# Kernel optimization log

Hardware: AMD Instinct MI355X
Metric: run time of the kernel (lower is better)

## Reference

```python
import jax, jax.numpy as jnp
import numpy as np

NODE_DIM, EDGE_DIM = 128, 64
N_NODES, N_EDGES = 50000, 500000
BN_EPS = 1e-5


def _glorot(key, shape):
    fan_in, fan_out = shape[0], shape[-1]
    s = np.sqrt(2.0 / (fan_in + fan_out)).astype(np.float32)
    return jax.random.normal(key, shape, jnp.float32) * s


def setup_inputs() -> dict:
    key = jax.random.key(0)
    ks = jax.random.split(key, 24)
    inp = {
        "x": jax.random.normal(ks[0], (N_NODES, NODE_DIM), jnp.float32),
        "edge_index": jax.random.randint(ks[1], (2, N_EDGES), 0, N_NODES),
        "edge_features": jax.random.normal(ks[2], (N_EDGES, EDGE_DIM), jnp.float32),
        "num_nodes": N_NODES,
        # CustomSAGEConv params (shared across the num_layers loop, as the module
        # instantiates a single self.conv)
        "W_nb": _glorot(ks[3], (NODE_DIM + EDGE_DIM, NODE_DIM)),
        "b_nb": jnp.zeros((NODE_DIM,), jnp.float32),
        "W_self": _glorot(ks[4], (NODE_DIM, NODE_DIM)),
        "b_self": jnp.zeros((NODE_DIM,), jnp.float32),
    }
    # MLP: 320 -> 512 -> 256 -> 128 -> 64 -> 32 -> 1, BN after first two linears
    dims = [2 * NODE_DIM + EDGE_DIM, 512, 256, 128, 64, 32, 1]
    for i in range(6):
        inp[f"W{i+1}"] = _glorot(ks[5 + i], (dims[i], dims[i + 1]))
        inp[f"b{i+1}"] = jnp.zeros((dims[i + 1],), jnp.float32)
    inp["g1"] = jnp.ones((512,), jnp.float32)
    inp["beta1"] = jnp.zeros((512,), jnp.float32)
    inp["g2"] = jnp.ones((256,), jnp.float32)
    inp["beta2"] = jnp.zeros((256,), jnp.float32)
    return inp


def _batchnorm(h, g, b):
    # training-mode batch statistics (deterministic reference)
    m = jnp.mean(h, axis=0)
    v = jnp.var(h, axis=0)
    return g * (h - m) * jax.lax.rsqrt(v + BN_EPS) + b


def _sage_conv(x, src, dst, ef, num_nodes, W_nb, b_nb, W_self, b_self):
    # message from source node + edge feature, mean-aggregated at destination
    msg = jnp.concatenate([x[src], ef], axis=-1) @ W_nb + b_nb  # [E, node_dim]
    deg = jax.ops.segment_sum(jnp.ones(src.shape[0], x.dtype), dst, num_segments=num_nodes)
    agg = jax.ops.segment_sum(msg, dst, num_segments=num_nodes) / jnp.clip(deg, 1.0)[:, None]
    return x @ W_self + b_self + agg


def reference(x, edge_index, edge_features, num_nodes,
              W_nb, b_nb, W_self, b_self,
              W1, b1, W2, b2, W3, b3, W4, b4, W5, b5, W6, b6,
              g1, beta1, g2, beta2):
    src, dst = edge_index[0], edge_index[1]
    num_layers = 2
    for _ in range(num_layers):
        x = _sage_conv(x, src, dst, edge_features, num_nodes, W_nb, b_nb, W_self, b_self)
        x = jax.nn.relu(x)  # dropout is identity in eval
    v, u = edge_index[0], edge_index[1]
    pair = jnp.concatenate([x[v], x[u], edge_features], axis=-1)  # [E, 320]
    h = jax.nn.relu(_batchnorm(pair @ W1 + b1, g1, beta1))
    h = jax.nn.relu(_batchnorm(h @ W2 + b2, g2, beta2))
    h = jax.nn.relu(h @ W3 + b3)
    h = jax.nn.relu(h @ W4 + b4)
    h = jax.nn.relu(h @ W5 + b5)
    return h @ W6 + b6  # [E, 1]
```

## Files before the change

kernel.cpp:

```cpp
#include <hip/hip_runtime.h>

using bf16 = __bf16;
typedef bf16 bf16x8 __attribute__((ext_vector_type(8)));
typedef float f32x4 __attribute__((ext_vector_type(4)));

#define MFMA16(a, b, c) __builtin_amdgcn_mfma_f32_16x16x32_bf16(a, b, c, 0, 0, 0)


__device__ __forceinline__ bf16x8 to_bf16x8(float4 a, float4 b) {
    bf16x8 v;
    v[0] = (bf16)a.x; v[1] = (bf16)a.y; v[2] = (bf16)a.z; v[3] = (bf16)a.w;
    v[4] = (bf16)b.x; v[5] = (bf16)b.y; v[6] = (bf16)b.z; v[7] = (bf16)b.w;
    return v;
}

__device__ __forceinline__ bf16x8 lds_afrag(const char* smem, int ldK, int mbase, int kbase, int lane) {
    int r = mbase + (lane & 15);
    int off = (kbase + ((lane >> 4) << 3)) << 1;
    off ^= (r & 7) << 4;
    return *(const bf16x8*)(smem + r * (ldK << 1) + off);
}

__device__ __forceinline__ bf16x8 glb_bfrag(const bf16* __restrict__ WT, int K, int nbase, int kbase, int lane) {
    int n = nbase + (lane & 15);
    int k = kbase + ((lane >> 4) << 3);
    return *(const bf16x8*)(WT + (size_t)n * K + k);
}


__global__ void k_transpose(const float* __restrict__ W, bf16* __restrict__ WT,
                            int K, int N, int ldT, int k0) {
    int idx = blockIdx.x * 256 + threadIdx.x;
    if (idx < K * N) {
        int k = idx / N, n = idx - k * N;
        WT[(size_t)n * ldT + k0 + k] = (bf16)W[idx];
    }
}

__global__ void k_deg(const int* __restrict__ dst, float* __restrict__ deg, int E) {
    int e = blockIdx.x * 256 + threadIdx.x;
    if (e < E) atomicAdd(&deg[dst[e]], 1.0f);
}

__global__ void k_scan(const float* __restrict__ deg, unsigned* __restrict__ offsets,
                       float* __restrict__ invdeg, int N) {
    __shared__ unsigned wsum[16];
    __shared__ unsigned carry_s, tot_s;
    const int tid = threadIdx.x, lane = tid & 63, wid = tid >> 6;
    if (tid == 0) carry_s = 0;
    __syncthreads();
    for (int base = 0; base < N; base += 1024) {
        int i = base + tid;
        unsigned v = (i < N) ? (unsigned)deg[i] : 0u;
        unsigned inc = v;
        #pragma unroll
        for (int d = 1; d < 64; d <<= 1) {
            unsigned t = (unsigned)__shfl_up((int)inc, d, 64);
            if (lane >= d) inc += t;
        }
        if (lane == 63) wsum[wid] = inc;
        __syncthreads();
        if (wid == 0) {
            unsigned wv = (lane < 16) ? wsum[lane] : 0u;
            unsigned winc = wv;
            #pragma unroll
            for (int d = 1; d < 16; d <<= 1) {
                unsigned t = (unsigned)__shfl_up((int)winc, d, 16);
                if ((lane & 15) >= d) winc += t;
            }
            if (lane < 16) wsum[lane] = winc - wv;
            if (lane == 15) tot_s = winc;
        }
        __syncthreads();
        if (i < N) {
            offsets[i] = carry_s + wsum[wid] + (inc - v);
            invdeg[i] = 1.0f / fmaxf(deg[i], 1.0f);
        }
        __syncthreads();
        if (tid == 0) carry_s += tot_s;
        __syncthreads();
    }
    if (tid == 0) offsets[N] = carry_s;
}

__global__ void k_scatter(const int* __restrict__ dst, const unsigned* __restrict__ offsets,
                          unsigned* __restrict__ cursor, unsigned* __restrict__ eid, int E) {
    int e = blockIdx.x * 256 + threadIdx.x;
    if (e < E) {
        int d = dst[e];
        unsigned p = atomicAdd(&cursor[d], 1u);
        eid[offsets[d] + p] = (unsigned)e;
    }
}

__global__ __launch_bounds__(256)
void k_agg(const float* __restrict__ xin, const float* __restrict__ ef, const int* __restrict__ src,
           const unsigned* __restrict__ offsets, const float* __restrict__ invdeg,
           const unsigned* __restrict__ eid, float* __restrict__ sm, int N) {
    const int lane = threadIdx.x & 63, w = threadIdx.x >> 6;
    int nb = blockIdx.x * 16 + w * 4;
    for (int j = 0; j < 4; ++j) {
        int n = nb + j;
        if (n >= N) return;
        unsigned o0 = offsets[n], o1 = offsets[n + 1];
        float s0 = 0.f, s1 = 0.f, s2 = 0.f;
        for (unsigned t = o0; t < o1; ++t) {
            int e = (int)eid[t];
            int v = src[e];
            s0 += xin[(size_t)v * 128 + lane];
            s1 += xin[(size_t)v * 128 + 64 + lane];
            s2 += ef[(size_t)e * 64 + lane];
        }
        float g = invdeg[n];
        sm[(size_t)n * 192 + lane] = s0 * g;
        sm[(size_t)n * 192 + 64 + lane] = s1 * g;
        sm[(size_t)n * 192 + 128 + lane] = s2 * g;
    }
}

__global__ __launch_bounds__(256)
void k_nodegemm(const float* __restrict__ xin, const float* __restrict__ sm,
                const bf16* __restrict__ WcatT,
                const float* __restrict__ b_self, const float* __restrict__ b_nb,
                const unsigned* __restrict__ offsets,
                float* __restrict__ xout, int N) {
    __shared__ char smem[64 * 320 * 2];
    const int tid = threadIdx.x, lane = tid & 63, w = tid >> 6;
    const int n0 = blockIdx.x * 64;
    for (int it = tid; it < 64 * 40; it += 256) {
        int r = it / 40, c = it - r * 40;
        int node = n0 + r;
        float4 fa = {0, 0, 0, 0}, fb = {0, 0, 0, 0};
        if (node < N) {
            int base = c * 8;
            const float* p = (base < 128) ? xin + (size_t)node * 128 + base
                                          : sm + (size_t)node * 192 + (base - 128);
            fa = *(const float4*)p;
            fb = *(const float4*)(p + 4);
        }
        bf16x8 v = to_bf16x8(fa, fb);
        *(bf16x8*)(smem + r * 640 + ((c * 16) ^ ((r & 7) << 4))) = v;
    }
    __syncthreads();

    f32x4 acc[4][2];
    #pragma unroll
    for (int m = 0; m < 4; ++m)
        #pragma unroll
        for (int n = 0; n < 2; ++n) acc[m][n] = (f32x4){0.f, 0.f, 0.f, 0.f};

    for (int ks = 0; ks < 10; ++ks) {
        bf16x8 a[4];
        #pragma unroll
        for (int m = 0; m < 4; ++m) a[m] = lds_afrag(smem, 320, m * 16, ks * 32, lane);
        #pragma unroll
        for (int n = 0; n < 2; ++n) {
            bf16x8 b = glb_bfrag(WcatT, 320, w * 32 + n * 16, ks * 32, lane);
            #pragma unroll
            for (int m = 0; m < 4; ++m) acc[m][n] = MFMA16(a[m], b, acc[m][n]);
        }
    }

    #pragma unroll
    for (int n = 0; n < 2; ++n) {
        int col = w * 32 + n * 16 + (lane & 15);
        float bs = b_self[col], bn = b_nb[col];
        #pragma unroll
        for (int m = 0; m < 4; ++m)
            #pragma unroll
            for (int rr = 0; rr < 4; ++rr) {
                int row = m * 16 + ((lane >> 4) << 2) + rr;
                int node = n0 + row;
                if (node < N) {
                    bool hd = offsets[node + 1] > offsets[node];
                    xout[(size_t)node * 128 + col] =
                        fmaxf(acc[m][n][rr] + bs + (hd ? bn : 0.f), 0.f);
                }
            }
    }
}

__global__ void k_finalize(const float* __restrict__ sum, const float* __restrict__ sq,
                           const float* __restrict__ g, const float* __restrict__ beta,
                           float* __restrict__ scale, float* __restrict__ shift,
                           int n, float invE) {
    int i = blockIdx.x * 256 + threadIdx.x;
    if (i < n) {
        float m = sum[i] * invE;
        float v = sq[i] * invE - m * m;
        float sc = g[i] * rsqrtf(v + 1e-5f);
        scale[i] = sc;
        shift[i] = beta[i] - m * sc;
    }
}

template <int PASS>
__global__ __launch_bounds__(256, 2)
void k_mlp(const float* __restrict__ x, const int* __restrict__ ei, const float* __restrict__ ef,
           const bf16* __restrict__ W1T, const float* __restrict__ b1,
           const bf16* __restrict__ W2T, const float* __restrict__ b2,
           const bf16* __restrict__ W3T, const float* __restrict__ b3,
           const bf16* __restrict__ W4T, const float* __restrict__ b4,
           const bf16* __restrict__ W5T, const float* __restrict__ b5,
           const float* __restrict__ W6, const float* __restrict__ b6,
           const float* __restrict__ scale1, const float* __restrict__ shift1,
           const float* __restrict__ scale2, const float* __restrict__ shift2,
           float* __restrict__ sum1, float* __restrict__ sq1,
           float* __restrict__ sum2, float* __restrict__ sq2,
           float* __restrict__ out, int E) {
    __shared__ char smem[65536];
    const int tid = threadIdx.x, lane = tid & 63, w = tid >> 6;
    const int e0 = blockIdx.x * 64;
    const int* src = ei;
    const int* dst = ei + E;

    for (int it = tid; it < 64 * 40; it += 256) {
        int r = it / 40, c = it - r * 40;
        int ge = e0 + r;
        float4 fa = {0, 0, 0, 0}, fb = {0, 0, 0, 0};
        if (ge < E) {
            int base = c * 8;
            const float* p;
            if (base < 128)      p = x + (size_t)src[ge] * 128 + base;
            else if (base < 256) p = x + (size_t)dst[ge] * 128 + (base - 128);
            else                 p = ef + (size_t)ge * 64 + (base - 256);
            fa = *(const float4*)p;
            fb = *(const float4*)(p + 4);
        }
        bf16x8 v = to_bf16x8(fa, fb);
        *(bf16x8*)(smem + r * 640 + ((c * 16) ^ ((r & 7) << 4))) = v;
    }
    __syncthreads();

    f32x4 acc[4][8];
    #pragma unroll
    for (int m = 0; m < 4; ++m)
        #pragma unroll
        for (int n = 0; n < 8; ++n) acc[m][n] = (f32x4){0.f, 0.f, 0.f, 0.f};
    #pragma unroll 2
    for (int ks = 0; ks < 10; ++ks) {
        bf16x8 a[4];
        #pragma unroll
        for (int m = 0; m < 4; ++m) a[m] = lds_afrag(smem, 320, m * 16, ks * 32, lane);
        #pragma unroll
        for (int n = 0; n < 8; ++n) {
            bf16x8 b = glb_bfrag(W1T, 320, w * 128 + n * 16, ks * 32, lane);
            #pragma unroll
            for (int m = 0; m < 4; ++m) acc[m][n] = MFMA16(a[m], b, acc[m][n]);
        }
    }
    const int cb = w * 128;

    if (PASS == 0) {
        #pragma unroll
        for (int n = 0; n < 8; ++n) {
            int col = cb + n * 16 + (lane & 15);
            float bb = b1[col];
            float s = 0.f, q = 0.f;
            #pragma unroll
            for (int m = 0; m < 4; ++m)
                #pragma unroll
                for (int rr = 0; rr < 4; ++rr) {
                    int row = m * 16 + ((lane >> 4) << 2) + rr;
                    if (e0 + row < E) {
                        float h = acc[m][n][rr] + bb;
                        s += h; q += h * h;
                    }
                }
            s += __shfl_xor(s, 16); s += __shfl_xor(s, 32);
            q += __shfl_xor(q, 16); q += __shfl_xor(q, 32);
            if (lane < 16) { atomicAdd(&sum1[col], s); atomicAdd(&sq1[col], q); }
        }
        return;
    }

    __syncthreads();
    #pragma unroll
    for (int n = 0; n < 8; ++n) {
        int col = cb + n * 16 + (lane & 15);
        float bb = b1[col], sc = scale1[col], sh = shift1[col];
        #pragma unroll
        for (int m = 0; m < 4; ++m)
            #pragma unroll
            for (int rr = 0; rr < 4; ++rr) {
                int row = m * 16 + ((lane >> 4) << 2) + rr;
                float a = fmaxf(fmaf(acc[m][n][rr] + bb, sc, sh), 0.f);
                int off = (col * 2) ^ ((row & 7) << 4);
                *(bf16*)(smem + row * 1024 + off) = (bf16)a;
            }
    }
    __syncthreads();

    f32x4 acc2[4][4];
    #pragma unroll
    for (int m = 0; m < 4; ++m)
        #pragma unroll
        for (int n = 0; n < 4; ++n) acc2[m][n] = (f32x4){0.f, 0.f, 0.f, 0.f};
    #pragma unroll 2
    for (int ks = 0; ks < 16; ++ks) {
        bf16x8 a[4];
        #pragma unroll
        for (int m = 0; m < 4; ++m) a[m] = lds_afrag(smem, 512, m * 16, ks * 32, lane);
        #pragma unroll
        for (int n = 0; n < 4; ++n) {
            bf16x8 b = glb_bfrag(W2T, 512, w * 64 + n * 16, ks * 32, lane);
            #pragma unroll
            for (int m = 0; m < 4; ++m) acc2[m][n] = MFMA16(a[m], b, acc2[m][n]);
        }
    }
    const int cb2 = w * 64;

    if (PASS == 1) {
        #pragma unroll
        for (int n = 0; n < 4; ++n) {
            int col = cb2 + n * 16 + (lane & 15);
            float bb = b2[col];
            float s = 0.f, q = 0.f;
            #pragma unroll
            for (int m = 0; m < 4; ++m)
                #pragma unroll
                for (int rr = 0; rr < 4; ++rr) {
                    int row = m * 16 + ((lane >> 4) << 2) + rr;
                    if (e0 + row < E) {
                        float h = acc2[m][n][rr] + bb;
                        s += h; q += h * h;
                    }
                }
            s += __shfl_xor(s, 16); s += __shfl_xor(s, 32);
            q += __shfl_xor(q, 16); q += __shfl_xor(q, 32);
            if (lane < 16) { atomicAdd(&sum2[col], s); atomicAdd(&sq2[col], q); }
        }
        return;
    }

    __syncthreads();
    if (tid < 32) *(float*)(smem + 49152 + tid * 4) = W6[tid];
    #pragma unroll
    for (int n = 0; n < 4; ++n) {
        int col = cb2 + n * 16 + (lane & 15);
        float bb = b2[col], sc = scale2[col], sh = shift2[col];
        #pragma unroll
        for (int m = 0; m < 4; ++m)
            #pragma unroll
            for (int rr = 0; rr < 4; ++rr) {
                int row = m * 16 + ((lane >> 4) << 2) + rr;
                float a = fmaxf(fmaf(acc2[m][n][rr] + bb, sc, sh), 0.f);
                int off = (col * 2) ^ ((row & 7) << 4);
                *(bf16*)(smem + row * 512 + off) = (bf16)a;
            }
    }
    __syncthreads();

    f32x4 acc3[4][2];
    #pragma unroll
    for (int m = 0; m < 4; ++m)
        #pragma unroll
        for (int n = 0; n < 2; ++n) acc3[m][n] = (f32x4){0.f, 0.f, 0.f, 0.f};
    for (int ks = 0; ks < 8; ++ks) {
        bf16x8 a[4];
        #pragma unroll
        for (int m = 0; m < 4; ++m) a[m] = lds_afrag(smem, 256, m * 16, ks * 32, lane);
        #pragma unroll
        for (int n = 0; n < 2; ++n) {
            bf16x8 b = glb_bfrag(W3T, 256, w * 32 + n * 16, ks * 32, lane);
            #pragma unroll
            for (int m = 0; m < 4; ++m) acc3[m][n] = MFMA16(a[m], b, acc3[m][n]);
        }
    }
    __syncthreads();
    #pragma unroll
    for (int n = 0; n < 2; ++n) {
        int col = w * 32 + n * 16 + (lane & 15);
        float bb = b3[col];
        #pragma unroll
        for (int m = 0; m < 4; ++m)
            #pragma unroll
            for (int rr = 0; rr < 4; ++rr) {
                int row = m * 16 + ((lane >> 4) << 2) + rr;
                float a = fmaxf(acc3[m][n][rr] + bb, 0.f);
                int off = (col * 2) ^ ((row & 7) << 4);
                *(bf16*)(smem + row * 256 + off) = (bf16)a;
            }
    }
    __syncthreads();

    f32x4 acc4[4];
    #pragma unroll
    for (int m = 0; m < 4; ++m) acc4[m] = (f32x4){0.f, 0.f, 0.f, 0.f};
    for (int ks = 0; ks < 4; ++ks) {
        bf16x8 a[4];
        #pragma unroll
        for (int m = 0; m < 4; ++m) a[m] = lds_afrag(smem, 128, m * 16, ks * 32, lane);
        bf16x8 b = glb_bfrag(W4T, 128, w * 16, ks * 32, lane);
        #pragma unroll
        for (int m = 0; m < 4; ++m) acc4[m] = MFMA16(a[m], b, acc4[m]);
    }
    __syncthreads();
    {
        int col = w * 16 + (lane & 15);
        float bb = b4[col];
        #pragma unroll
        for (int m = 0; m < 4; ++m)
            #pragma unroll
            for (int rr = 0; rr < 4; ++rr) {
                int row = m * 16 + ((lane >> 4) << 2) + rr;
                float a = fmaxf(acc4[m][rr] + bb, 0.f);
                int off = (col * 2) ^ ((row & 7) << 4);
                *(bf16*)(smem + row * 128 + off) = (bf16)a;
            }
    }
    __syncthreads();

    if (w < 2) {
        f32x4 acc5[4];
        #pragma unroll
        for (int m = 0; m < 4; ++m) acc5[m] = (f32x4){0.f, 0.f, 0.f, 0.f};
        for (int ks = 0; ks < 2; ++ks) {
            bf16x8 a[4];
            #pragma unroll
            for (int m = 0; m < 4; ++m) a[m] = lds_afrag(smem, 64, m * 16, ks * 32, lane);
            bf16x8 b = glb_bfrag(W5T, 64, w * 16, ks * 32, lane);
            #pragma unroll
            for (int m = 0; m < 4; ++m) acc5[m] = MFMA16(a[m], b, acc5[m]);
        }
        int col = w * 16 + (lane & 15);
        float bb = b5[col];
        float* a5f = (float*)(smem + 16384);
        #pragma unroll
        for (int m = 0; m < 4; ++m)
            #pragma unroll
            for (int rr = 0; rr < 4; ++rr) {
                int row = m * 16 + ((lane >> 4) << 2) + rr;
                a5f[row * 32 + col] = fmaxf(acc5[m][rr] + bb, 0.f);
            }
    }
    __syncthreads();

    if (tid < 64) {
        int ge = e0 + tid;
        if (ge < E) {
            const float* a5f = (const float*)(smem + 16384) + tid * 32;
            const float* w6 = (const float*)(smem + 49152);
            float s = b6[0];
            #pragma unroll
            for (int k = 0; k < 32; ++k) {
                int kk = (k + tid) & 31;
                s = fmaf(a5f[kk], w6[kk], s);
            }
            out[ge] = s;
        }
    }
}


extern "C" void kernel_launch(void* const* d_in, const int* in_sizes, int n_in,
                              void* d_out, int out_size, void* d_ws, size_t ws_size,
                              hipStream_t stream) {
    const float* x      = (const float*)d_in[0];
    const int*   ei     = (const int*)d_in[1];
    const float* ef     = (const float*)d_in[2];
    const float* W_nb   = (const float*)d_in[4];
    const float* b_nb   = (const float*)d_in[5];
    const float* W_self = (const float*)d_in[6];
    const float* b_self = (const float*)d_in[7];
    const float* W1 = (const float*)d_in[8];  const float* b1 = (const float*)d_in[9];
    const float* W2 = (const float*)d_in[10]; const float* b2 = (const float*)d_in[11];
    const float* W3 = (const float*)d_in[12]; const float* b3 = (const float*)d_in[13];
    const float* W4 = (const float*)d_in[14]; const float* b4 = (const float*)d_in[15];
    const float* W5 = (const float*)d_in[16]; const float* b5 = (const float*)d_in[17];
    const float* W6 = (const float*)d_in[18]; const float* b6 = (const float*)d_in[19];
    const float* g1 = (const float*)d_in[20]; const float* beta1 = (const float*)d_in[21];
    const float* g2 = (const float*)d_in[22]; const float* beta2 = (const float*)d_in[23];

    const int N = in_sizes[0] / 128;
    const int E = in_sizes[1] / 2;

    char* ws = (char*)d_ws;
    size_t off = 0;
    auto alloc = [&](size_t bytes) {
        size_t o = off;
        off = (off + bytes + 255) & ~(size_t)255;
        return o;
    };
    size_t oDeg = alloc((size_t)N * 4);
    size_t oCur = alloc((size_t)N * 4);
    size_t oSum1 = alloc(512 * 4), oSq1 = alloc(512 * 4);
    size_t oSum2 = alloc(256 * 4), oSq2 = alloc(256 * 4);
    size_t zeroEnd = off;
    size_t oOff = alloc((size_t)(N + 1) * 4);
    size_t oInv = alloc((size_t)N * 4);
    size_t oEid = alloc((size_t)E * 4);
    size_t oSm  = alloc((size_t)N * 192 * 4);
    size_t oXb1 = alloc((size_t)N * 128 * 4);
    size_t oXb2 = alloc((size_t)N * 128 * 4);
    size_t oScale1 = alloc(512 * 4), oShift1 = alloc(512 * 4);
    size_t oScale2 = alloc(256 * 4), oShift2 = alloc(256 * 4);
    size_t oWcat = alloc(128 * 320 * 2);
    size_t oW1T = alloc((size_t)512 * 320 * 2);
    size_t oW2T = alloc((size_t)256 * 512 * 2);
    size_t oW3T = alloc((size_t)128 * 256 * 2);
    size_t oW4T = alloc((size_t)64 * 128 * 2);
    size_t oW5T = alloc((size_t)32 * 64 * 2);
    if (ws_size < off) return;

    float* deg = (float*)(ws + oDeg);
    unsigned* cursor = (unsigned*)(ws + oCur);
    float* sum1 = (float*)(ws + oSum1); float* sq1 = (float*)(ws + oSq1);
    float* sum2 = (float*)(ws + oSum2); float* sq2 = (float*)(ws + oSq2);
    unsigned* offsets = (unsigned*)(ws + oOff);
    float* invdeg = (float*)(ws + oInv);
    unsigned* eid = (unsigned*)(ws + oEid);
    float* sm  = (float*)(ws + oSm);
    float* xb1 = (float*)(ws + oXb1);
    float* xb2 = (float*)(ws + oXb2);
    float* scale1 = (float*)(ws + oScale1); float* shift1 = (float*)(ws + oShift1);
    float* scale2 = (float*)(ws + oScale2); float* shift2 = (float*)(ws + oShift2);
    bf16* WcatT = (bf16*)(ws + oWcat);
    bf16* W1T = (bf16*)(ws + oW1T);
    bf16* W2T = (bf16*)(ws + oW2T);
    bf16* W3T = (bf16*)(ws + oW3T);
    bf16* W4T = (bf16*)(ws + oW4T);
    bf16* W5T = (bf16*)(ws + oW5T);

    hipMemsetAsync(ws, 0, zeroEnd, stream);

    k_transpose<<<(128 * 128 + 255) / 256, 256, 0, stream>>>(W_self, WcatT, 128, 128, 320, 0);
    k_transpose<<<(192 * 128 + 255) / 256, 256, 0, stream>>>(W_nb, WcatT, 192, 128, 320, 128);
    k_transpose<<<(320 * 512 + 255) / 256, 256, 0, stream>>>(W1, W1T, 320, 512, 320, 0);
    k_transpose<<<(512 * 256 + 255) / 256, 256, 0, stream>>>(W2, W2T, 512, 256, 512, 0);
    k_transpose<<<(256 * 128 + 255) / 256, 256, 0, stream>>>(W3, W3T, 256, 128, 256, 0);
    k_transpose<<<(128 * 64 + 255) / 256, 256, 0, stream>>>(W4, W4T, 128, 64, 128, 0);
    k_transpose<<<(64 * 32 + 255) / 256, 256, 0, stream>>>(W5, W5T, 64, 32, 64, 0);

    const int* dst = ei + E;
    k_deg<<<(E + 255) / 256, 256, 0, stream>>>(dst, deg, E);
    k_scan<<<1, 1024, 0, stream>>>(deg, offsets, invdeg, N);
    k_scatter<<<(E + 255) / 256, 256, 0, stream>>>(dst, offsets, cursor, eid, E);

    k_agg<<<(N + 15) / 16, 256, 0, stream>>>(x, ef, ei, offsets, invdeg, eid, sm, N);
    k_nodegemm<<<(N + 63) / 64, 256, 0, stream>>>(x, sm, WcatT, b_self, b_nb, offsets, xb1, N);
    k_agg<<<(N + 15) / 16, 256, 0, stream>>>(xb1, ef, ei, offsets, invdeg, eid, sm, N);
    k_nodegemm<<<(N + 63) / 64, 256, 0, stream>>>(xb1, sm, WcatT, b_self, b_nb, offsets, xb2, N);

    const float invE = 1.0f / (float)E;
    const int mlpGrid = (E + 63) / 64;
    k_mlp<0><<<mlpGrid, 256, 0, stream>>>(xb2, ei, ef, W1T, b1, W2T, b2, W3T, b3, W4T, b4,
                                          W5T, b5, W6, b6, scale1, shift1, scale2, shift2,
                                          sum1, sq1, sum2, sq2, (float*)d_out, E);
    k_finalize<<<2, 256, 0, stream>>>(sum1, sq1, g1, beta1, scale1, shift1, 512, invE);
    k_mlp<1><<<mlpGrid, 256, 0, stream>>>(xb2, ei, ef, W1T, b1, W2T, b2, W3T, b3, W4T, b4,
                                          W5T, b5, W6, b6, scale1, shift1, scale2, shift2,
                                          sum1, sq1, sum2, sq2, (float*)d_out, E);
    k_finalize<<<1, 256, 0, stream>>>(sum2, sq2, g2, beta2, scale2, shift2, 256, invE);
    k_mlp<2><<<mlpGrid, 256, 0, stream>>>(xb2, ei, ef, W1T, b1, W2T, b2, W3T, b3, W4T, b4,
                                          W5T, b5, W6, b6, scale1, shift1, scale2, shift2,
                                          sum1, sq1, sum2, sq2, (float*)d_out, E);
}
```

Before: 2.611 ms.

## Materialize pair features and pre-BN H2 to skip recomputation across MLP passes

The first MLP pass now writes the gathered bf16 pair matrix to a workspace buffer, so later passes stream it contiguously instead of re-gathering node rows. When enough workspace is available, the second pass also stores pre-BN layer-2 activations in fp32, so the final pass skips both GEMM1 and GEMM2 and starts from layer 3. The second-layer A operand is staged in two halves to cut shared memory to 40KB and allow 4 blocks per CU. The cost is extra global traffic (about 320MB for pair plus 512MB for h2 written and read back), and which path runs depends on the workspace size.

```diff
diff --git a/kernel.cpp b/kernel.cpp
--- a/kernel.cpp
+++ b/kernel.cpp
@@ -194,6 +194,386 @@
     }
 }
 
+
+__device__ __forceinline__ void run_gemm1(const char* smem, const bf16* __restrict__ W1T,
+                                          int w, int lane, f32x4 (&acc)[4][8]) {
+    #pragma unroll
+    for (int m = 0; m < 4; ++m)
+        #pragma unroll
+        for (int n = 0; n < 8; ++n) acc[m][n] = (f32x4){0.f, 0.f, 0.f, 0.f};
+    #pragma unroll 2
+    for (int ks = 0; ks < 10; ++ks) {
+        bf16x8 a[4];
+        #pragma unroll
+        for (int m = 0; m < 4; ++m) a[m] = lds_afrag(smem, 320, m * 16, ks * 32, lane);
+        #pragma unroll
+        for (int n = 0; n < 8; ++n) {
+            bf16x8 b = glb_bfrag(W1T, 320, w * 128 + n * 16, ks * 32, lane);
+            #pragma unroll
+            for (int m = 0; m < 4; ++m) acc[m][n] = MFMA16(a[m], b, acc[m][n]);
+        }
+    }
+}
+
+__device__ __forceinline__ void stage_pair_glb(char* smem, const bf16* __restrict__ pairG,
+                                               int e0, int tid) {
+    for (int it = tid; it < 64 * 40; it += 256) {
+        int r = it / 40, c = it - r * 40;
+        bf16x8 v = *(const bf16x8*)(pairG + (size_t)(e0 + r) * 320 + c * 8);
+        *(bf16x8*)(smem + r * 640 + ((c * 16) ^ ((r & 7) << 4))) = v;
+    }
+}
+
+__device__ __forceinline__ void write_a1_chunk(char* a1buf, const f32x4 (&acc)[4][8], int w, int lane,
+                                               const float* __restrict__ b1,
+                                               const float* __restrict__ scale1,
+                                               const float* __restrict__ shift1) {
+    const int cb = w * 128;
+    #pragma unroll
+    for (int n = 0; n < 8; ++n) {
+        int col = cb + n * 16 + (lane & 15);
+        int colc = col & 255;
+        float bb = b1[col], sc = scale1[col], sh = shift1[col];
+        #pragma unroll
+        for (int m = 0; m < 4; ++m)
+            #pragma unroll
+            for (int rr = 0; rr < 4; ++rr) {
+                int row = m * 16 + ((lane >> 4) << 2) + rr;
+                float a = fmaxf(fmaf(acc[m][n][rr] + bb, sc, sh), 0.f);
+                *(bf16*)(a1buf + row * 512 + ((colc * 2) ^ ((row & 7) << 4))) = (bf16)a;
+            }
+    }
+}
+
+__device__ __forceinline__ void gemm2_half(const char* a1buf, const bf16* __restrict__ W2T,
+                                           int w, int lane, int kg0, f32x4 (&acc2)[4][4]) {
+    #pragma unroll 2
+    for (int ks = 0; ks < 8; ++ks) {
+        bf16x8 a[4];
+        #pragma unroll
+        for (int m = 0; m < 4; ++m) a[m] = lds_afrag(a1buf, 256, m * 16, ks * 32, lane);
+        #pragma unroll
+        for (int n = 0; n < 4; ++n) {
+            bf16x8 b = glb_bfrag(W2T, 512, w * 64 + n * 16, kg0 + ks * 32, lane);
+            #pragma unroll
+            for (int m = 0; m < 4; ++m) acc2[m][n] = MFMA16(a[m], b, acc2[m][n]);
+        }
+    }
+}
+
+__device__ __forceinline__ void mlp_tail(char* smem,
+                                         const bf16* __restrict__ W3T, const float* __restrict__ b3,
+                                         const bf16* __restrict__ W4T, const float* __restrict__ b4,
+                                         const bf16* __restrict__ W5T, const float* __restrict__ b5,
+                                         const float* __restrict__ W6, const float* __restrict__ b6,
+                                         float* __restrict__ out, int E, int e0,
+                                         int tid, int lane, int w) {
+    f32x4 acc3[4][2];
+    #pragma unroll
+    for (int m = 0; m < 4; ++m)
+        #pragma unroll
+        for (int n = 0; n < 2; ++n) acc3[m][n] = (f32x4){0.f, 0.f, 0.f, 0.f};
+    for (int ks = 0; ks < 8; ++ks) {
+        bf16x8 a[4];
+        #pragma unroll
+        for (int m = 0; m < 4; ++m) a[m] = lds_afrag(smem, 256, m * 16, ks * 32, lane);
+        #pragma unroll
+        for (int n = 0; n < 2; ++n) {
+            bf16x8 b = glb_bfrag(W3T, 256, w * 32 + n * 16, ks * 32, lane);
+            #pragma unroll
+            for (int m = 0; m < 4; ++m) acc3[m][n] = MFMA16(a[m], b, acc3[m][n]);
+        }
+    }
+    __syncthreads();
+    if (tid < 32) ((float*)(smem + 24576))[tid] = W6[tid];
+    #pragma unroll
+    for (int n = 0; n < 2; ++n) {
+        int col = w * 32 + n * 16 + (lane & 15);
+        float bb = b3[col];
+        #pragma unroll
+        for (int m = 0; m < 4; ++m)
+            #pragma unroll
+            for (int rr = 0; rr < 4; ++rr) {
+                int row = m * 16 + ((lane >> 4) << 2) + rr;
+                float a = fmaxf(acc3[m][n][rr] + bb, 0.f);
+                *(bf16*)(smem + row * 256 + ((col * 2) ^ ((row & 7) << 4))) = (bf16)a;
+            }
+    }
+    __syncthreads();
+
+    f32x4 acc4[4];
+    #pragma unroll
+    for (int m = 0; m < 4; ++m) acc4[m] = (f32x4){0.f, 0.f, 0.f, 0.f};
+    for (int ks = 0; ks < 4; ++ks) {
+        bf16x8 a[4];
+        #pragma unroll
+        for (int m = 0; m < 4; ++m) a[m] = lds_afrag(smem, 128, m * 16, ks * 32, lane);
+        bf16x8 b = glb_bfrag(W4T, 128, w * 16, ks * 32, lane);
+        #pragma unroll
+        for (int m = 0; m < 4; ++m) acc4[m] = MFMA16(a[m], b, acc4[m]);
+    }
+    __syncthreads();
+    {
+        int col = w * 16 + (lane & 15);
+        float bb = b4[col];
+        #pragma unroll
+        for (int m = 0; m < 4; ++m)
+            #pragma unroll
+            for (int rr = 0; rr < 4; ++rr) {
+                int row = m * 16 + ((lane >> 4) << 2) + rr;
+                float a = fmaxf(acc4[m][rr] + bb, 0.f);
+                *(bf16*)(smem + row * 128 + ((col * 2) ^ ((row & 7) << 4))) = (bf16)a;
+            }
+    }
+    __syncthreads();
+
+    if (w < 2) {
+        f32x4 acc5[4];
+        #pragma unroll
+        for (int m = 0; m < 4; ++m) acc5[m] = (f32x4){0.f, 0.f, 0.f, 0.f};
+        for (int ks = 0; ks < 2; ++ks) {
+            bf16x8 a[4];
+            #pragma unroll
+            for (int m = 0; m < 4; ++m) a[m] = lds_afrag(smem, 64, m * 16, ks * 32, lane);
+            bf16x8 b = glb_bfrag(W5T, 64, w * 16, ks * 32, lane);
+            #pragma unroll
+            for (int m = 0; m < 4; ++m) acc5[m] = MFMA16(a[m], b, acc5[m]);
+        }
+        int col = w * 16 + (lane & 15);
+        float bb = b5[col];
+        float* a5f = (float*)(smem + 16384);
+        #pragma unroll
+        for (int m = 0; m < 4; ++m)
+            #pragma unroll
+            for (int rr = 0; rr < 4; ++rr) {
+                int row = m * 16 + ((lane >> 4) << 2) + rr;
+                a5f[row * 32 + col] = fmaxf(acc5[m][rr] + bb, 0.f);
+            }
+    }
+    __syncthreads();
+
+    if (tid < 64) {
+        int ge = e0 + tid;
+        if (ge < E) {
+            const float* a5f = (const float*)(smem + 16384) + tid * 32;
+            const float* w6 = (const float*)(smem + 24576);
+            float s = b6[0];
+            #pragma unroll
+            for (int k = 0; k < 32; ++k) {
+                int kk = (k + tid) & 31;
+                s = fmaf(a5f[kk], w6[kk], s);
+            }
+            out[ge] = s;
+        }
+    }
+}
+
+
+__global__ __launch_bounds__(256, 4)
+void k_mlpA(const float* __restrict__ x, const int* __restrict__ ei, const float* __restrict__ ef,
+            const bf16* __restrict__ W1T, const float* __restrict__ b1,
+            float* __restrict__ sum1, float* __restrict__ sq1,
+            bf16* __restrict__ pairG, int E) {
+    __shared__ char smem[40960];
+    const int tid = threadIdx.x, lane = tid & 63, w = tid >> 6;
+    const int e0 = blockIdx.x * 64;
+    const int* src = ei;
+    const int* dst = ei + E;
+
+    for (int it = tid; it < 64 * 40; it += 256) {
+        int r = it / 40, c = it - r * 40;
+        int ge = e0 + r;
+        float4 fa = {0, 0, 0, 0}, fb = {0, 0, 0, 0};
+        if (ge < E) {
+            int base = c * 8;
+            const float* p;
+            if (base < 128)      p = x + (size_t)src[ge] * 128 + base;
+            else if (base < 256) p = x + (size_t)dst[ge] * 128 + (base - 128);
+            else                 p = ef + (size_t)ge * 64 + (base - 256);
+            fa = *(const float4*)p;
+            fb = *(const float4*)(p + 4);
+        }
+        bf16x8 v = to_bf16x8(fa, fb);
+        *(bf16x8*)(smem + r * 640 + ((c * 16) ^ ((r & 7) << 4))) = v;
+        *(bf16x8*)(pairG + (size_t)ge * 320 + c * 8) = v;
+    }
+    __syncthreads();
+
+    f32x4 acc[4][8];
+    run_gemm1(smem, W1T, w, lane, acc);
+
+    const int cb = w * 128;
+    #pragma unroll
+    for (int n = 0; n < 8; ++n) {
+        int col = cb + n * 16 + (lane & 15);
+        float bb = b1[col];
+        float s = 0.f, q = 0.f;
+        #pragma unroll
+        for (int m = 0; m < 4; ++m)
+            #pragma unroll
+            for (int rr = 0; rr < 4; ++rr) {
+                int row = m * 16 + ((lane >> 4) << 2) + rr;
+                if (e0 + row < E) {
+                    float h = acc[m][n][rr] + bb;
+                    s += h; q += h * h;
+                }
+            }
+        s += __shfl_xor(s, 16); s += __shfl_xor(s, 32);
+        q += __shfl_xor(q, 16); q += __shfl_xor(q, 32);
+        if (lane < 16) { atomicAdd(&sum1[col], s); atomicAdd(&sq1[col], q); }
+    }
+}
+
+template <int STORE_H2>
+__global__ __launch_bounds__(256, 4)
+void k_mlpB(const bf16* __restrict__ pairG,
+            const bf16* __restrict__ W1T, const float* __restrict__ b1,
+            const bf16* __restrict__ W2T, const float* __restrict__ b2,
+            const float* __restrict__ scale1, const float* __restrict__ shift1,
+            float* __restrict__ sum2, float* __restrict__ sq2,
+            float* __restrict__ h2G, int E) {
+    __shared__ char smem[40960];
+    const int tid = threadIdx.x, lane = tid & 63, w = tid >> 6;
+    const int e0 = blockIdx.x * 64;
+
+    stage_pair_glb(smem, pairG, e0, tid);
+    __syncthreads();
+
+    f32x4 acc[4][8];
+    run_gemm1(smem, W1T, w, lane, acc);
+    __syncthreads();
+
+    char* a1buf = smem;
+    f32x4 acc2[4][4];
+    #pragma unroll
+    for (int m = 0; m < 4; ++m)
+        #pragma unroll
+        for (int n = 0; n < 4; ++n) acc2[m][n] = (f32x4){0.f, 0.f, 0.f, 0.f};
+
+    if (w < 2) write_a1_chunk(a1buf, acc, w, lane, b1, scale1, shift1);
+    __syncthreads();
+    gemm2_half(a1buf, W2T, w, lane, 0, acc2);
+    __syncthreads();
+    if (w >= 2) write_a1_chunk(a1buf, acc, w, lane, b1, scale1, shift1);
+    __syncthreads();
+    gemm2_half(a1buf, W2T, w, lane, 256, acc2);
+
+    const int cb2 = w * 64;
+    #pragma unroll
+    for (int n = 0; n < 4; ++n) {
+        int col = cb2 + n * 16 + (lane & 15);
+        float bb = b2[col];
+        float s = 0.f, q = 0.f;
+        #pragma unroll
+        for (int m = 0; m < 4; ++m)
+            #pragma unroll
+            for (int rr = 0; rr < 4; ++rr) {
+                int row = m * 16 + ((lane >> 4) << 2) + rr;
+                float h = acc2[m][n][rr] + bb;
+                if (STORE_H2) h2G[(size_t)(e0 + row) * 256 + col] = h;
+                if (e0 + row < E) { s += h; q += h * h; }
+            }
+        s += __shfl_xor(s, 16); s += __shfl_xor(s, 32);
+        q += __shfl_xor(q, 16); q += __shfl_xor(q, 32);
+        if (lane < 16) { atomicAdd(&sum2[col], s); atomicAdd(&sq2[col], q); }
+    }
+}
+
+__global__ __launch_bounds__(256, 4)
+void k_mlpC_h2(const float* __restrict__ h2G,
+               const bf16* __restrict__ W3T, const float* __restrict__ b3,
+               const bf16* __restrict__ W4T, const float* __restrict__ b4,
+               const bf16* __restrict__ W5T, const float* __restrict__ b5,
+               const float* __restrict__ W6, const float* __restrict__ b6,
+               const float* __restrict__ scale2, const float* __restrict__ shift2,
+               float* __restrict__ out, int E) {
+    __shared__ char smem[32768];
+    const int tid = threadIdx.x, lane = tid & 63, w = tid >> 6;
+    const int e0 = blockIdx.x * 64;
+
+    for (int it = tid; it < 64 * 32; it += 256) {
+        int r = it >> 5, c = it & 31;
+        const float* p = h2G + (size_t)(e0 + r) * 256 + c * 8;
+        float4 fa = *(const float4*)p;
+        float4 fb = *(const float4*)(p + 4);
+        float4 s0 = *(const float4*)(scale2 + c * 8);
+        float4 s1 = *(const float4*)(scale2 + c * 8 + 4);
+        float4 h0 = *(const float4*)(shift2 + c * 8);
+        float4 h1 = *(const float4*)(shift2 + c * 8 + 4);
+        float4 ra, rb;
+        ra.x = fmaxf(fmaf(fa.x, s0.x, h0.x), 0.f);
+        ra.y = fmaxf(fmaf(fa.y, s0.y, h0.y), 0.f);
+        ra.z = fmaxf(fmaf(fa.z, s0.z, h0.z), 0.f);
+        ra.w = fmaxf(fmaf(fa.w, s0.w, h0.w), 0.f);
+        rb.x = fmaxf(fmaf(fb.x, s1.x, h1.x), 0.f);
+        rb.y = fmaxf(fmaf(fb.y, s1.y, h1.y), 0.f);
+        rb.z = fmaxf(fmaf(fb.z, s1.z, h1.z), 0.f);
+        rb.w = fmaxf(fmaf(fb.w, s1.w, h1.w), 0.f);
+        bf16x8 v = to_bf16x8(ra, rb);
+        *(bf16x8*)(smem + r * 512 + ((c * 16) ^ ((r & 7) << 4))) = v;
+    }
+    __syncthreads();
+
+    mlp_tail(smem, W3T, b3, W4T, b4, W5T, b5, W6, b6, out, E, e0, tid, lane, w);
+}
+
+__global__ __launch_bounds__(256, 4)
+void k_mlpC_pair(const bf16* __restrict__ pairG,
+                 const bf16* __restrict__ W1T, const float* __restrict__ b1,
+                 const bf16* __restrict__ W2T, const float* __restrict__ b2,
+                 const bf16* __restrict__ W3T, const float* __restrict__ b3,
+                 const bf16* __restrict__ W4T, const float* __restrict__ b4,
+                 const bf16* __restrict__ W5T, const float* __restrict__ b5,
+                 const float* __restrict__ W6, const float* __restrict__ b6,
+                 const float* __restrict__ scale1, const float* __restrict__ shift1,
+                 const float* __restrict__ scale2, const float* __restrict__ shift2,
+                 float* __restrict__ out, int E) {
+    __shared__ char smem[40960];
+    const int tid = threadIdx.x, lane = tid & 63, w = tid >> 6;
+    const int e0 = blockIdx.x * 64;
+
+    stage_pair_glb(smem, pairG, e0, tid);
+    __syncthreads();
+
+    f32x4 acc[4][8];
+    run_gemm1(smem, W1T, w, lane, acc);
+    __syncthreads();
+
+    char* a1buf = smem;
+    f32x4 acc2[4][4];
+    #pragma unroll
+    for (int m = 0; m < 4; ++m)
+        #pragma unroll
+        for (int n = 0; n < 4; ++n) acc2[m][n] = (f32x4){0.f, 0.f, 0.f, 0.f};
+
+    if (w < 2) write_a1_chunk(a1buf, acc, w, lane, b1, scale1, shift1);
+    __syncthreads();
+    gemm2_half(a1buf, W2T, w, lane, 0, acc2);
+    __syncthreads();
+    if (w >= 2) write_a1_chunk(a1buf, acc, w, lane, b1, scale1, shift1);
+    __syncthreads();
+    gemm2_half(a1buf, W2T, w, lane, 256, acc2);
+    __syncthreads();
+
+    const int cb2 = w * 64;
+    #pragma unroll
+    for (int n = 0; n < 4; ++n) {
+        int col = cb2 + n * 16 + (lane & 15);
+        float bb = b2[col], sc = scale2[col], sh = shift2[col];
+        #pragma unroll
+        for (int m = 0; m < 4; ++m)
+            #pragma unroll
+            for (int rr = 0; rr < 4; ++rr) {
+                int row = m * 16 + ((lane >> 4) << 2) + rr;
+                float a = fmaxf(fmaf(acc2[m][n][rr] + bb, sc, sh), 0.f);
+                *(bf16*)(smem + row * 512 + ((col * 2) ^ ((row & 7) << 4))) = (bf16)a;
+            }
+    }
+    __syncthreads();
+
+    mlp_tail(smem, W3T, b3, W4T, b4, W5T, b5, W6, b6, out, E, e0, tid, lane, w);
+}
+
 template <int PASS>
 __global__ __launch_bounds__(256, 2)
 void k_mlp(const float* __restrict__ x, const int* __restrict__ ei, const float* __restrict__ ef,
@@ -233,22 +613,7 @@
     __syncthreads();
 
     f32x4 acc[4][8];
-    #pragma unroll
-    for (int m = 0; m < 4; ++m)
-        #pragma unroll
-        for (int n = 0; n < 8; ++n) acc[m][n] = (f32x4){0.f, 0.f, 0.f, 0.f};
-    #pragma unroll 2
-    for (int ks = 0; ks < 10; ++ks) {
-        bf16x8 a[4];
-        #pragma unroll
-        for (int m = 0; m < 4; ++m) a[m] = lds_afrag(smem, 320, m * 16, ks * 32, lane);
-        #pragma unroll
-        for (int n = 0; n < 8; ++n) {
-            bf16x8 b = glb_bfrag(W1T, 320, w * 128 + n * 16, ks * 32, lane);
-            #pragma unroll
-            for (int m = 0; m < 4; ++m) acc[m][n] = MFMA16(a[m], b, acc[m][n]);
-        }
-    }
+    run_gemm1(smem, W1T, w, lane, acc);
     const int cb = w * 128;
 
     if (PASS == 0) {
@@ -285,8 +650,7 @@
             for (int rr = 0; rr < 4; ++rr) {
                 int row = m * 16 + ((lane >> 4) << 2) + rr;
                 float a = fmaxf(fmaf(acc[m][n][rr] + bb, sc, sh), 0.f);
-                int off = (col * 2) ^ ((row & 7) << 4);
-                *(bf16*)(smem + row * 1024 + off) = (bf16)a;
+                *(bf16*)(smem + row * 1024 + ((col * 2) ^ ((row & 7) << 4))) = (bf16)a;
             }
     }
     __syncthreads();
@@ -345,8 +709,7 @@
             for (int rr = 0; rr < 4; ++rr) {
                 int row = m * 16 + ((lane >> 4) << 2) + rr;
                 float a = fmaxf(fmaf(acc2[m][n][rr] + bb, sc, sh), 0.f);
-                int off = (col * 2) ^ ((row & 7) << 4);
-                *(bf16*)(smem + row * 512 + off) = (bf16)a;
+                *(bf16*)(smem + row * 512 + ((col * 2) ^ ((row & 7) << 4))) = (bf16)a;
             }
     }
     __syncthreads();
@@ -378,8 +741,7 @@
             for (int rr = 0; rr < 4; ++rr) {
                 int row = m * 16 + ((lane >> 4) << 2) + rr;
                 float a = fmaxf(acc3[m][n][rr] + bb, 0.f);
-                int off = (col * 2) ^ ((row & 7) << 4);
-                *(bf16*)(smem + row * 256 + off) = (bf16)a;
+                *(bf16*)(smem + row * 256 + ((col * 2) ^ ((row & 7) << 4))) = (bf16)a;
             }
     }
     __syncthreads();
@@ -405,8 +767,7 @@
             for (int rr = 0; rr < 4; ++rr) {
                 int row = m * 16 + ((lane >> 4) << 2) + rr;
                 float a = fmaxf(acc4[m][rr] + bb, 0.f);
-                int off = (col * 2) ^ ((row & 7) << 4);
-                *(bf16*)(smem + row * 128 + off) = (bf16)a;
+                *(bf16*)(smem + row * 128 + ((col * 2) ^ ((row & 7) << 4))) = (bf16)a;
             }
     }
     __syncthreads();
@@ -474,6 +835,8 @@
 
     const int N = in_sizes[0] / 128;
     const int E = in_sizes[1] / 2;
+    const int mlpGrid = (E + 63) / 64;
+    const size_t Epad = (size_t)mlpGrid * 64;
 
     char* ws = (char*)d_ws;
     size_t off = 0;
@@ -501,7 +864,14 @@
     size_t oW3T = alloc((size_t)128 * 256 * 2);
     size_t oW4T = alloc((size_t)64 * 128 * 2);
     size_t oW5T = alloc((size_t)32 * 64 * 2);
-    if (ws_size < off) return;
+    size_t baseEnd = off;
+    size_t oPair = alloc(Epad * 320 * 2);
+    size_t pairEnd = off;
+    size_t oH2 = alloc(Epad * 256 * 4);
+    size_t fullEnd = off;
+
+    int mode = (ws_size >= fullEnd) ? 2 : (ws_size >= pairEnd) ? 1 : (ws_size >= baseEnd) ? 0 : -1;
+    if (mode < 0) return;
 
     float* deg = (float*)(ws + oDeg);
     unsigned* cursor = (unsigned*)(ws + oCur);
@@ -521,6 +891,8 @@
     bf16* W3T = (bf16*)(ws + oW3T);
     bf16* W4T = (bf16*)(ws + oW4T);
     bf16* W5T = (bf16*)(ws + oW5T);
+    bf16* pairG = (bf16*)(ws + oPair);
+    float* h2G = (float*)(ws + oH2);
 
     hipMemsetAsync(ws, 0, zeroEnd, stream);
 
@@ -543,16 +915,34 @@
     k_nodegemm<<<(N + 63) / 64, 256, 0, stream>>>(xb1, sm, WcatT, b_self, b_nb, offsets, xb2, N);
 
     const float invE = 1.0f / (float)E;
-    const int mlpGrid = (E + 63) / 64;
-    k_mlp<0><<<mlpGrid, 256, 0, stream>>>(xb2, ei, ef, W1T, b1, W2T, b2, W3T, b3, W4T, b4,
-                                          W5T, b5, W6, b6, scale1, shift1, scale2, shift2,
-                                          sum1, sq1, sum2, sq2, (float*)d_out, E);
-    k_finalize<<<2, 256, 0, stream>>>(sum1, sq1, g1, beta1, scale1, shift1, 512, invE);
-    k_mlp<1><<<mlpGrid, 256, 0, stream>>>(xb2, ei, ef, W1T, b1, W2T, b2, W3T, b3, W4T, b4,
-                                          W5T, b5, W6, b6, scale1, shift1, scale2, shift2,
-                                          sum1, sq1, sum2, sq2, (float*)d_out, E);
-    k_finalize<<<1, 256, 0, stream>>>(sum2, sq2, g2, beta2, scale2, shift2, 256, invE);
-    k_mlp<2><<<mlpGrid, 256, 0, stream>>>(xb2, ei, ef, W1T, b1, W2T, b2, W3T, b3, W4T, b4,
-                                          W5T, b5, W6, b6, scale1, shift1, scale2, shift2,
-                                          sum1, sq1, sum2, sq2, (float*)d_out, E);
-}
+    if (mode >= 1) {
+        k_mlpA<<<mlpGrid, 256, 0, stream>>>(xb2, ei, ef, W1T, b1, sum1, sq1, pairG, E);
+        k_finalize<<<2, 256, 0, stream>>>(sum1, sq1, g1, beta1, scale1, shift1, 512, invE);
+        if (mode == 2) {
+            k_mlpB<1><<<mlpGrid, 256, 0, stream>>>(pairG, W1T, b1, W2T, b2, scale1, shift1,
+                                                   sum2, sq2, h2G, E);
+            k_finalize<<<1, 256, 0, stream>>>(sum2, sq2, g2, beta2, scale2, shift2, 256, invE);
+            k_mlpC_h2<<<mlpGrid, 256, 0, stream>>>(h2G, W3T, b3, W4T, b4, W5T, b5, W6, b6,
+                                                   scale2, shift2, (float*)d_out, E);
+        } else {
+            k_mlpB<0><<<mlpGrid, 256, 0, stream>>>(pairG, W1T, b1, W2T, b2, scale1, shift1,
+                                                   sum2, sq2, h2G, E);
+            k_finalize<<<1, 256, 0, stream>>>(sum2, sq2, g2, beta2, scale2, shift2, 256, invE);
+            k_mlpC_pair<<<mlpGrid, 256, 0, stream>>>(pairG, W1T, b1, W2T, b2, W3T, b3, W4T, b4,
+                                                     W5T, b5, W6, b6, scale1, shift1,
+                                                     scale2, shift2, (float*)d_out, E);
+        }
+    } else {
+        k_mlp<0><<<mlpGrid, 256, 0, stream>>>(xb2, ei, ef, W1T, b1, W2T, b2, W3T, b3, W4T, b4,
+                                              W5T, b5, W6, b6, scale1, shift1, scale2, shift2,
+                                              sum1, sq1, sum2, sq2, (float*)d_out, E);
+        k_finalize<<<2, 256, 0, stream>>>(sum1, sq1, g1, beta1, scale1, shift1, 512, invE);
+        k_mlp<1><<<mlpGrid, 256, 0, stream>>>(xb2, ei, ef, W1T, b1, W2T, b2, W3T, b3, W4T, b4,
+                                              W5T, b5, W6, b6, scale1, shift1, scale2, shift2,
+                                              sum1, sq1, sum2, sq2, (float*)d_out, E);
+        k_finalize<<<1, 256, 0, stream>>>(sum2, sq2, g2, beta2, scale2, shift2, 256, invE);
+        k_mlp<2><<<mlpGrid, 256, 0, stream>>>(xb2, ei, ef, W1T, b1, W2T, b2, W3T, b3, W4T, b4,
+                                              W5T, b5, W6, b6, scale1, shift1, scale2, shift2,
+                                              sum1, sq1, sum2, sq2, (float*)d_out, E);
+    }
+}
```

New measurement: 6.042 ms. +131.4%, slower.
